# Performance work log

Measured on AMD Instinct MI355X. Metric: run time of the kernel, lower is better.

Reference implementation:

```python
import jax, jax.numpy as jnp
import numpy as np

DIM = 512
HEADS = 16
WS = 8          # window size
SHIFT = 4       # shift size
POSMLP = 32
MLP_HID = 4 * DIM
B = 32
HH = 56
WW = 56
EPS = 1e-5


def setup_inputs() -> dict:
    key = jax.random.key(0)
    ks = jax.random.split(key, 20)
    s = 0.02
    inp = {
        'x': jax.random.normal(ks[0], (B, HH * WW, DIM), jnp.float32),
        'g1': jnp.ones((DIM,), jnp.float32),
        'be1': jnp.zeros((DIM,), jnp.float32),
        'w_qkv': s * jax.random.normal(ks[1], (3 * DIM, DIM), jnp.float32),
        'b_qkv': jnp.zeros((3 * DIM,), jnp.float32),
        'pm_w1': s * jax.random.normal(ks[2], (POSMLP, 2), jnp.float32),
        'pm_b1': jnp.zeros((POSMLP,), jnp.float32),
        'pm_w2': s * jax.random.normal(ks[3], (HEADS, POSMLP), jnp.float32),
        'pm_b2': jnp.zeros((HEADS,), jnp.float32),
        'w_proj': s * jax.random.normal(ks[4], (DIM, DIM), jnp.float32),
        'b_proj': jnp.zeros((DIM,), jnp.float32),
        'g2': jnp.ones((DIM,), jnp.float32),
        'be2': jnp.zeros((DIM,), jnp.float32),
        'w_fc1': s * jax.random.normal(ks[5], (MLP_HID, DIM), jnp.float32),
        'b_fc1': jnp.zeros((MLP_HID,), jnp.float32),
        'w_fc2': s * jax.random.normal(ks[6], (DIM, MLP_HID), jnp.float32),
        'b_fc2': jnp.zeros((DIM,), jnp.float32),
        'H': HH,
        'W': WW,
    }
    return inp


def _layernorm(x, g, b):
    m = jnp.mean(x, -1, keepdims=True)
    v = jnp.mean(jnp.square(x - m), -1, keepdims=True)
    return (x - m) * jax.lax.rsqrt(v + EPS) * g + b


def _shift_mask(H, W, ws, sh):
    # static numpy construction of the (nW, N, N) 0/-100 shift mask
    img = np.zeros((H, W), np.float32)
    cnt = 0
    for hs in (slice(0, -ws), slice(-ws, -sh), slice(-sh, None)):
        for wsl in (slice(0, -ws), slice(-ws, -sh), slice(-sh, None)):
            img[hs, wsl] = cnt
            cnt += 1
    mw = img.reshape(H // ws, ws, W // ws, ws).transpose(0, 2, 1, 3).reshape(-1, ws * ws)
    diff = mw[:, None, :] - mw[:, :, None]
    return jnp.asarray(np.where(diff != 0, -100.0, 0.0).astype(np.float32))


def _pos_bias(ws, pm_w1, pm_b1, pm_w2, pm_b2):
    # log-CPB relative position bias computed by a tiny MLP -> (heads, N, N)
    g = jnp.stack(jnp.meshgrid(jnp.arange(ws), jnp.arange(ws), indexing='ij'))
    coords = g.reshape(2, -1).astype(jnp.float32)        # [2, N]
    d = coords[:, :, None] - coords[:, None, :]          # [2, N, N]
    d = jnp.sign(d) * jnp.log1p(jnp.abs(d))
    h = jax.nn.relu(jnp.einsum('cnm,oc->onm', d, pm_w1) + pm_b1[:, None, None])
    return jnp.einsum('onm,ho->hnm', h, pm_w2) + pm_b2[:, None, None]


def reference(x, g1, be1, w_qkv, b_qkv, pm_w1, pm_b1, pm_w2, pm_b2,
              w_proj, b_proj, g2, be2, w_fc1, b_fc1, w_fc2, b_fc2, H, W):
    ws, sh, nh = WS, SHIFT, HEADS
    Bb, L, C = x.shape
    hd = C // nh
    scale = hd ** -0.5
    N = ws * ws
    nWh, nWw = H // ws, W // ws
    nW = nWh * nWw

    shortcut = x
    xn = _layernorm(x, g1, be1).reshape(Bb, H, W, C)
    xn = jnp.roll(xn, (-sh, -sh), axis=(1, 2))
    # window partition -> (B*nW, N, C)
    xw = xn.reshape(Bb, nWh, ws, nWw, ws, C).transpose(0, 1, 3, 2, 4, 5).reshape(-1, N, C)

    qkv = (xw @ w_qkv.T + b_qkv).reshape(-1, N, 3, nh, hd).transpose(2, 0, 3, 1, 4)
    q, k, v = qkv[0], qkv[1], qkv[2]           # each (B*nW, nh, N, hd)

    attn = jnp.einsum('bhnd,bhmd->bhnm', q * scale, k)
    attn = attn + _pos_bias(ws, pm_w1, pm_b1, pm_w2, pm_b2)[None]

    mask = _shift_mask(H, W, ws, sh)           # (nW, N, N)
    attn = attn.reshape(Bb, nW, nh, N, N) + mask[None, :, None]
    attn = jax.nn.softmax(attn.reshape(-1, nh, N, N), axis=-1)

    out = jnp.einsum('bhnm,bhmd->bhnd', attn, v).transpose(0, 2, 1, 3).reshape(-1, N, C)
    out = out @ w_proj.T + b_proj

    # window reverse + roll back
    out = out.reshape(Bb, nWh, nWw, ws, ws, C).transpose(0, 1, 3, 2, 4, 5).reshape(Bb, H, W, C)
    out = jnp.roll(out, (sh, sh), axis=(1, 2)).reshape(Bb, L, C)

    x1 = shortcut + out
    h = jax.nn.gelu(_layernorm(x1, g2, be2) @ w_fc1.T + b_fc1, approximate=False)
    return x1 + (h @ w_fc2.T + b_fc2)
```

## Files before the change

### kernel.cpp

```cpp
#include <hip/hip_runtime.h>
#include <math.h>

typedef __bf16 bf16;
typedef bf16 bf16x8 __attribute__((ext_vector_type(8)));
typedef float f32x4 __attribute__((ext_vector_type(4)));

#define MFMA_BF16(a, b, c) __builtin_amdgcn_mfma_f32_16x16x32_bf16((a), (b), (c), 0, 0, 0)
#define GLDS16(gp, lp)                                                            \
  __builtin_amdgcn_global_load_lds((__attribute__((address_space(1))) void*)(gp), \
                                   (__attribute__((address_space(3))) void*)(lp), 16, 0, 0)
#define VMCNT4 asm volatile("s_waitcnt vmcnt(4)" ::: "memory")
#define LGKM0 asm volatile("s_waitcnt lgkmcnt(0)" ::: "memory")
#define SBAR __builtin_amdgcn_s_barrier()
#define SCHED0 __builtin_amdgcn_sched_barrier(0)

static constexpr int kDim   = 512;
static constexpr int kHeads = 16;
static constexpr int kHd    = 32;
static constexpr int kNt    = 64;
static constexpr int kNw    = 49;
static constexpr int kL     = 3136;
static constexpr int kToks  = 100352;
static constexpr int kWins  = 1568;
static constexpr int kHid   = 2048;
static constexpr size_t kQS = (size_t)kWins * kHeads * kNt * kHd;

__global__ __launch_bounds__(256) void wconv_kernel(const float* __restrict__ s,
                                                    bf16* __restrict__ d, int n8) {
  int i = blockIdx.x * 256 + threadIdx.x;
  if (i >= n8) return;
  const float4 a = *(const float4*)(s + i * 8);
  const float4 b = *(const float4*)(s + i * 8 + 4);
  bf16x8 o;
  o[0] = (bf16)a.x; o[1] = (bf16)a.y; o[2] = (bf16)a.z; o[3] = (bf16)a.w;
  o[4] = (bf16)b.x; o[5] = (bf16)b.y; o[6] = (bf16)b.z; o[7] = (bf16)b.w;
  *(bf16x8*)(d + i * 8) = o;
}

__global__ void posbias_kernel(const float* __restrict__ w1, const float* __restrict__ b1,
                               const float* __restrict__ w2, const float* __restrict__ b2,
                               float* __restrict__ tbl) {
  int idx = blockIdx.x * 256 + threadIdx.x;
  if (idx >= kHeads * kNt * kNt) return;
  int h = idx >> 12, n = (idx >> 6) & 63, m = idx & 63;
  float dr = (float)((n >> 3) - (m >> 3));
  float dc = (float)((n & 7) - (m & 7));
  dr = (dr > 0.f ? 1.f : (dr < 0.f ? -1.f : 0.f)) * log1pf(fabsf(dr));
  dc = (dc > 0.f ? 1.f : (dc < 0.f ? -1.f : 0.f)) * log1pf(fabsf(dc));
  float acc = b2[h];
  for (int o = 0; o < 32; ++o) {
    float hv = w1[o * 2] * dr + w1[o * 2 + 1] * dc + b1[o];
    acc += w2[h * 32 + o] * fmaxf(hv, 0.f);
  }
  tbl[idx] = acc;
}

template <int MODE>
__global__ __launch_bounds__(256) void ln_kernel(const float* __restrict__ x,
                                                 const float* __restrict__ g,
                                                 const float* __restrict__ be,
                                                 bf16* __restrict__ o) {
  const int t = blockIdx.x * 4 + (threadIdx.x >> 6);
  const int lane = threadIdx.x & 63;
  size_t src;
  if (MODE == 0) {
    const int win = t >> 6, n = t & 63;
    const int b = win / kNw, wi = win % kNw;
    const int h0 = ((wi / 7) * 8 + (n >> 3) + 4) % 56;
    const int w0 = ((wi % 7) * 8 + (n & 7) + 4) % 56;
    src = ((size_t)b * kL + h0 * 56 + w0) * kDim;
  } else {
    src = (size_t)t * kDim;
  }
  const float4 a = *(const float4*)(x + src + lane * 8);
  const float4 bq = *(const float4*)(x + src + lane * 8 + 4);
  float xf[8] = {a.x, a.y, a.z, a.w, bq.x, bq.y, bq.z, bq.w};
  float s = 0.f, s2 = 0.f;
#pragma unroll
  for (int j = 0; j < 8; ++j) { s += xf[j]; s2 += xf[j] * xf[j]; }
#pragma unroll
  for (int off = 32; off > 0; off >>= 1) { s += __shfl_xor(s, off); s2 += __shfl_xor(s2, off); }
  const float mean = s * (1.f / 512.f);
  const float rstd = rsqrtf(s2 * (1.f / 512.f) - mean * mean + 1e-5f);
  const float4 ga = *(const float4*)(g + lane * 8);
  const float4 gb = *(const float4*)(g + lane * 8 + 4);
  const float4 ba = *(const float4*)(be + lane * 8);
  const float4 bb = *(const float4*)(be + lane * 8 + 4);
  const float gv[8] = {ga.x, ga.y, ga.z, ga.w, gb.x, gb.y, gb.z, gb.w};
  const float bv[8] = {ba.x, ba.y, ba.z, ba.w, bb.x, bb.y, bb.z, bb.w};
  bf16x8 ov;
#pragma unroll
  for (int j = 0; j < 8; ++j) ov[j] = (bf16)((xf[j] - mean) * rstd * gv[j] + bv[j]);
  *(bf16x8*)(o + (size_t)t * kDim + lane * 8) = ov;
}

#define READ_A(KH, MB)                                             \
  _Pragma("unroll") for (int i = 0; i < 4; ++i)                    \
      af[i] = *(const bf16x8*)(&L[cb][0][KH][aoff + (MB + i) * 512]);
#define READ_B(KH)                                                 \
  _Pragma("unroll") for (int i = 0; i < 4; ++i)                    \
      bfr[i] = *(const bf16x8*)(&L[cb][1][KH][boff + i * 512]);
#define MFMAS(MB)                                                  \
  LGKM0;                                                           \
  SCHED0;                                                          \
  __builtin_amdgcn_s_setprio(1);                                   \
  _Pragma("unroll") for (int mi = 0; mi < 4; ++mi)                 \
  _Pragma("unroll") for (int ni = 0; ni < 4; ++ni)                 \
      acc[MB + mi][ni] = MFMA_BF16(af[mi], bfr[ni], acc[MB + mi][ni]); \
  __builtin_amdgcn_s_setprio(0)

template <int EPI>
__global__ __launch_bounds__(512, 1) void gemm256(const bf16* __restrict__ A, const bf16* __restrict__ B,
                                                  const float* __restrict__ bias, void* __restrict__ Cv,
                                                  const float* __restrict__ extra, int N, int K) {
  __shared__ __align__(16) bf16 L[2][2][2][8192];
  const int nbn = N >> 8;
  const int nwg = (int)gridDim.x;
  int wg = (int)blockIdx.x;
  {
    const int q = nwg >> 3, r = nwg & 7;
    const int xcd = wg & 7, loc = wg >> 3;
    wg = (xcd < r ? xcd * (q + 1) : r * (q + 1) + (xcd - r) * q) + loc;
  }
  const int bm = wg / nbn, bn = wg % nbn;
  const int tid = (int)threadIdx.x;
  const int wave = tid >> 6, lane = tid & 63;
  const int wm2 = wave >> 2, wn4 = wave & 3;
  const int quad = lane >> 4, l16 = lane & 15;

  const int sl0 = tid, sl1 = 512 + tid;
  const int rp0 = sl0 >> 3, ls0 = (sl0 & 7) ^ (rp0 & 7);
  const int rp1 = sl1 >> 3, ls1 = (sl1 & 7) ^ (rp1 & 7);
  const int row0 = rp0 * 2 + (ls0 >> 2), c0 = ls0 & 3;
  const int row1 = rp1 * 2 + (ls1 >> 2), c1 = ls1 & 3;
  const bf16* pa0 = A + (size_t)(bm * 256 + row0) * K + c0 * 8;
  const bf16* pa1 = A + (size_t)(bm * 256 + row1) * K + c1 * 8;
  const bf16* pb0 = B + (size_t)(bn * 256 + row0) * K + c0 * 8;
  const bf16* pb1 = B + (size_t)(bn * 256 + row1) * K + c1 * 8;

  const int ar = wm2 * 128 + l16, arp = ar >> 1;
  const int aoff = (arp * 8 + ((((ar & 1) << 2) | quad) ^ (arp & 7))) * 8;
  const int br = wn4 * 64 + l16, brp = br >> 1;
  const int boff = (brp * 8 + ((((br & 1) << 2) | quad) ^ (brp & 7))) * 8;

  f32x4 acc[8][4] = {};
  bf16x8 af[4], bfr[4];

  GLDS16(pa0, &L[0][0][0][sl0 * 8]);
  GLDS16(pa1, &L[0][0][0][sl1 * 8]);
  GLDS16(pb0, &L[0][1][0][sl0 * 8]);
  GLDS16(pb1, &L[0][1][0][sl1 * 8]);
  GLDS16(pa0 + 32, &L[0][0][1][sl0 * 8]);
  GLDS16(pa1 + 32, &L[0][0][1][sl1 * 8]);
  GLDS16(pb0 + 32, &L[0][1][1][sl0 * 8]);
  GLDS16(pb1 + 32, &L[0][1][1][sl1 * 8]);
  VMCNT4;
  SBAR;

#pragma unroll 2
  for (int kt = 0; kt < K; kt += 64) {
    const int cb = (kt >> 6) & 1, nb = cb ^ 1;
    const int kn = (kt + 64 < K) ? (kt + 64) : kt;
    READ_A(0, 0);
    READ_B(0);
    GLDS16(pa0 + kn, &L[nb][0][0][sl0 * 8]);
    GLDS16(pa1 + kn, &L[nb][0][0][sl1 * 8]);
    SBAR;
    MFMAS(0);
    SBAR;
    READ_A(0, 4);
    GLDS16(pb0 + kn, &L[nb][1][0][sl0 * 8]);
    GLDS16(pb1 + kn, &L[nb][1][0][sl1 * 8]);
    SBAR;
    MFMAS(4);
    VMCNT4;
    SBAR;
    READ_A(1, 0);
    READ_B(1);
    GLDS16(pa0 + kn + 32, &L[nb][0][1][sl0 * 8]);
    GLDS16(pa1 + kn + 32, &L[nb][0][1][sl1 * 8]);
    SBAR;
    MFMAS(0);
    SBAR;
    READ_A(1, 4);
    GLDS16(pb0 + kn + 32, &L[nb][1][1][sl0 * 8]);
    GLDS16(pb1 + kn + 32, &L[nb][1][1][sl1 * 8]);
    SBAR;
    MFMAS(4);
    VMCNT4;
    SBAR;
  }

  bf16* Cb = (bf16*)Cv;
  float* Cf = (float*)Cv;
#pragma unroll
  for (int mi = 0; mi < 8; ++mi) {
#pragma unroll
    for (int ni = 0; ni < 4; ++ni) {
      const int col = bn * 256 + wn4 * 64 + ni * 16 + l16;
      const float bb = bias[col];
#pragma unroll
      for (int r = 0; r < 4; ++r) {
        const int row = bm * 256 + wm2 * 128 + mi * 16 + quad * 4 + r;
        float val = acc[mi][ni][r] + bb;
        if constexpr (EPI == 1) {
          const int which = col >> 9, head = (col >> 5) & 15, d = col & 31;
          const int win = row >> 6, n = row & 63;
          Cb[(size_t)which * kQS + (((size_t)win * kHeads + head) * kNt + n) * kHd + d] = (bf16)val;
        } else if constexpr (EPI == 2) {
          val = 0.5f * val * (1.f + erff(val * 0.70710678118654752f));
          Cb[(size_t)row * N + col] = (bf16)val;
        } else if constexpr (EPI == 3) {
          Cf[(size_t)row * N + col] = val + extra[(size_t)row * N + col];
        } else {
          const int win = row >> 6, n = row & 63;
          const int b = win / kNw, wi = win % kNw;
          const int h0 = ((wi / 7) * 8 + (n >> 3) + 4) % 56;
          const int w0 = ((wi % 7) * 8 + (n & 7) + 4) % 56;
          const size_t dst = ((size_t)b * kL + h0 * 56 + w0) * kDim + col;
          Cf[dst] = val + extra[dst];
        }
      }
    }
  }
}

__device__ __forceinline__ int reg3(int x) { return x < 48 ? 0 : (x < 52 ? 1 : 2); }

__global__ __launch_bounds__(128) void attn_kernel(const bf16* __restrict__ qkv,
                                                   const float* __restrict__ ptbl,
                                                   bf16* __restrict__ out) {
  __shared__ float Sb[2][64 * 65];
  __shared__ float Rs[2][64];
  __shared__ bf16  Pb[2][64 * 72];
  __shared__ bf16  Vt[2][32 * 72];
  const int w = threadIdx.x >> 6, lane = threadIdx.x & 63;
  const int gwh = blockIdx.x * 2 + w;
  const int win = gwh >> 4, h = gwh & 15;
  const int quad = lane >> 4, l16 = lane & 15;
  const bf16* q = qkv + ((size_t)win * kHeads + h) * (kNt * kHd);
  const bf16* k = q + kQS;
  const bf16* v = q + 2 * kQS;

#pragma unroll
  for (int i = 0; i < 4; ++i) {
    const int row = i * 16 + (lane >> 2);
    const int d0 = (lane & 3) * 8;
    bf16x8 vv = *(const bf16x8*)(v + row * kHd + d0);
#pragma unroll
    for (int j = 0; j < 8; ++j) Vt[w][(d0 + j) * 72 + row] = vv[j];
  }

  bf16x8 qf[4], kf[4];
#pragma unroll
  for (int i = 0; i < 4; ++i) qf[i] = *(const bf16x8*)(q + (i * 16 + l16) * kHd + quad * 8);
#pragma unroll
  for (int j = 0; j < 4; ++j) kf[j] = *(const bf16x8*)(k + (j * 16 + l16) * kHd + quad * 8);
  f32x4 sa[4][4] = {};
#pragma unroll
  for (int i = 0; i < 4; ++i)
#pragma unroll
    for (int j = 0; j < 4; ++j) sa[i][j] = MFMA_BF16(qf[i], kf[j], sa[i][j]);

  const int wi = win % kNw;
  const int hb = (wi / 7) * 8, wb = (wi % 7) * 8;
  const float* bh = ptbl + h * 4096;
#pragma unroll
  for (int i = 0; i < 4; ++i) {
#pragma unroll
    for (int j = 0; j < 4; ++j) {
      const int ct = j * 16 + l16;
      const int crg = reg3(hb + (ct >> 3)) * 3 + reg3(wb + (ct & 7));
#pragma unroll
      for (int r = 0; r < 4; ++r) {
        const int rt = i * 16 + quad * 4 + r;
        const int rrg = reg3(hb + (rt >> 3)) * 3 + reg3(wb + (rt & 7));
        float sv = sa[i][j][r] * 0.17677669529663687f + bh[rt * 64 + ct];
        if (rrg != crg) sv -= 100.f;
        Sb[w][rt * 65 + ct] = sv;
      }
    }
  }
  __syncthreads();

  float mx = -1e30f;
  for (int i = 0; i < 64; ++i) mx = fmaxf(mx, Sb[w][lane * 65 + i]);
  float sum = 0.f;
  for (int i = 0; i < 64; ++i) {
    const float p = __expf(Sb[w][lane * 65 + i] - mx);
    sum += p;
    Pb[w][lane * 72 + i] = (bf16)p;
  }
  Rs[w][lane] = 1.f / sum;
  __syncthreads();

  f32x4 oa[4][2] = {};
#pragma unroll
  for (int kk = 0; kk < 2; ++kk) {
    bf16x8 pf[4], vf[2];
#pragma unroll
    for (int mi = 0; mi < 4; ++mi)
      pf[mi] = *(const bf16x8*)(&Pb[w][(mi * 16 + l16) * 72 + kk * 32 + quad * 8]);
#pragma unroll
    for (int nj = 0; nj < 2; ++nj)
      vf[nj] = *(const bf16x8*)(&Vt[w][(nj * 16 + l16) * 72 + kk * 32 + quad * 8]);
#pragma unroll
    for (int mi = 0; mi < 4; ++mi)
#pragma unroll
      for (int nj = 0; nj < 2; ++nj) oa[mi][nj] = MFMA_BF16(pf[mi], vf[nj], oa[mi][nj]);
  }
#pragma unroll
  for (int mi = 0; mi < 4; ++mi)
#pragma unroll
    for (int nj = 0; nj < 2; ++nj)
#pragma unroll
      for (int r = 0; r < 4; ++r) {
        const int row = mi * 16 + quad * 4 + r;
        const int col = nj * 16 + l16;
        out[((size_t)win * kNt + row) * kDim + h * kHd + col] = (bf16)(oa[mi][nj][r] * Rs[w][row]);
      }
}

extern "C" void kernel_launch(void* const* d_in, const int* in_sizes, int n_in,
                              void* d_out, int out_size, void* d_ws, size_t ws_size,
                              hipStream_t stream) {
  (void)in_sizes; (void)n_in; (void)out_size; (void)ws_size;
  const float* x      = (const float*)d_in[0];
  const float* g1     = (const float*)d_in[1];
  const float* be1    = (const float*)d_in[2];
  const float* w_qkv  = (const float*)d_in[3];
  const float* b_qkv  = (const float*)d_in[4];
  const float* pm_w1  = (const float*)d_in[5];
  const float* pm_b1  = (const float*)d_in[6];
  const float* pm_w2  = (const float*)d_in[7];
  const float* pm_b2  = (const float*)d_in[8];
  const float* w_proj = (const float*)d_in[9];
  const float* b_proj = (const float*)d_in[10];
  const float* g2     = (const float*)d_in[11];
  const float* be2    = (const float*)d_in[12];
  const float* w_fc1  = (const float*)d_in[13];
  const float* b_fc1  = (const float*)d_in[14];
  const float* w_fc2  = (const float*)d_in[15];
  const float* b_fc2  = (const float*)d_in[16];
  float* out = (float*)d_out;
  char* ws = (char*)d_ws;

  constexpr size_t OFF_WB   = 1u << 20;
  constexpr size_t OFF_XW   = OFF_WB + (8u << 20);
  constexpr size_t SZ_ACT   = (size_t)kToks * kDim * 2;
  constexpr size_t OFF_QKV  = OFF_XW + SZ_ACT;
  float* biastbl = (float*)ws;
  bf16* wqb = (bf16*)(ws + OFF_WB);
  bf16* wpb = wqb + 786432;
  bf16* w1b = wpb + 262144;
  bf16* w2b = w1b + 1048576;
  bf16* xw    = (bf16*)(ws + OFF_XW);
  bf16* attnb = xw;
  bf16* xn2   = xw;
  bf16* qkvb = (bf16*)(ws + OFF_QKV);
  float* x1  = (float*)(ws + OFF_QKV);
  bf16* hbuf = (bf16*)(ws + OFF_QKV + (size_t)kToks * kDim * 4);

  wconv_kernel<<<dim3(786432 / 2048), dim3(256), 0, stream>>>(w_qkv, wqb, 786432 / 8);
  wconv_kernel<<<dim3(262144 / 2048), dim3(256), 0, stream>>>(w_proj, wpb, 262144 / 8);
  wconv_kernel<<<dim3(1048576 / 2048), dim3(256), 0, stream>>>(w_fc1, w1b, 1048576 / 8);
  wconv_kernel<<<dim3(1048576 / 2048), dim3(256), 0, stream>>>(w_fc2, w2b, 1048576 / 8);
  posbias_kernel<<<dim3(256), dim3(256), 0, stream>>>(pm_w1, pm_b1, pm_w2, pm_b2, biastbl);
  ln_kernel<0><<<dim3(kToks / 4), dim3(256), 0, stream>>>(x, g1, be1, xw);
  gemm256<1><<<dim3((kToks / 256) * (1536 / 256)), dim3(512), 0, stream>>>(
      xw, wqb, b_qkv, qkvb, nullptr, 1536, 512);
  attn_kernel<<<dim3(kWins * kHeads / 2), dim3(128), 0, stream>>>(qkvb, biastbl, attnb);
  gemm256<4><<<dim3((kToks / 256) * (512 / 256)), dim3(512), 0, stream>>>(
      attnb, wpb, b_proj, x1, x, 512, 512);
  ln_kernel<1><<<dim3(kToks / 4), dim3(256), 0, stream>>>(x1, g2, be2, xn2);
  constexpr int kChunk = kToks / 4;
  for (int c = 0; c < 4; ++c) {
    const size_t ro = (size_t)c * kChunk * kDim;
    gemm256<2><<<dim3((kChunk / 256) * (kHid / 256)), dim3(512), 0, stream>>>(
        xn2 + ro, w1b, b_fc1, hbuf, nullptr, kHid, 512);
    gemm256<3><<<dim3((kChunk / 256) * (512 / 256)), dim3(512), 0, stream>>>(
        hbuf, w2b, b_fc2, out + ro, x1 + ro, 512, kHid);
  }
}
```

Baseline: 1.660 ms.

## Double-buffer GEMM register fragments and relax waits to overlap LDS reads with MFMA

Restructures the 256x256 GEMM main loop so LDS fragment reads for the next MFMA group are issued before the current group runs, using two register sets and partial lgkmcnt/vmcnt waits instead of full drains. Several barriers are removed to cut stalls between the LDS reads and the MFMA work. It also changes launch bounds to request two workgroups per CU, which limits registers per thread and risks spills. The finer-grained waits also add risk that some data hazard has been overlooked.

```diff
diff --git a/kernel.cpp b/kernel.cpp
--- a/kernel.cpp
+++ b/kernel.cpp
@@ -9,8 +9,8 @@
 #define GLDS16(gp, lp)                                                            \
   __builtin_amdgcn_global_load_lds((__attribute__((address_space(1))) void*)(gp), \
                                    (__attribute__((address_space(3))) void*)(lp), 16, 0, 0)
-#define VMCNT4 asm volatile("s_waitcnt vmcnt(4)" ::: "memory")
-#define LGKM0 asm volatile("s_waitcnt lgkmcnt(0)" ::: "memory")
+#define VMCNT(N) asm volatile("s_waitcnt vmcnt(" #N ")" ::: "memory")
+#define LGKM(N) asm volatile("s_waitcnt lgkmcnt(" #N ")" ::: "memory")
 #define SBAR __builtin_amdgcn_s_barrier()
 #define SCHED0 __builtin_amdgcn_sched_barrier(0)
 
@@ -94,23 +94,22 @@
   *(bf16x8*)(o + (size_t)t * kDim + lane * 8) = ov;
 }
 
-#define READ_A(KH, MB)                                             \
-  _Pragma("unroll") for (int i = 0; i < 4; ++i)                    \
-      af[i] = *(const bf16x8*)(&L[cb][0][KH][aoff + (MB + i) * 512]);
-#define READ_B(KH)                                                 \
-  _Pragma("unroll") for (int i = 0; i < 4; ++i)                    \
-      bfr[i] = *(const bf16x8*)(&L[cb][1][KH][boff + i * 512]);
-#define MFMAS(MB)                                                  \
-  LGKM0;                                                           \
-  SCHED0;                                                          \
-  __builtin_amdgcn_s_setprio(1);                                   \
-  _Pragma("unroll") for (int mi = 0; mi < 4; ++mi)                 \
-  _Pragma("unroll") for (int ni = 0; ni < 4; ++ni)                 \
-      acc[MB + mi][ni] = MFMA_BF16(af[mi], bfr[ni], acc[MB + mi][ni]); \
+#define LOAD_A(dst, CB, KH, MB)                                        \
+  _Pragma("unroll") for (int i = 0; i < 4; ++i)                        \
+      dst[i] = *(const bf16x8*)(&L[CB][0][KH][aoff + (MB + i) * 512]);
+#define LOAD_B(dst, CB, KH)                                            \
+  _Pragma("unroll") for (int i = 0; i < 4; ++i)                        \
+      dst[i] = *(const bf16x8*)(&L[CB][1][KH][boff + i * 512]);
+#define MFMAS(MB, AF, BF)                                              \
+  SCHED0;                                                              \
+  __builtin_amdgcn_s_setprio(1);                                       \
+  _Pragma("unroll") for (int mi = 0; mi < 4; ++mi)                     \
+  _Pragma("unroll") for (int ni = 0; ni < 4; ++ni)                     \
+      acc[MB + mi][ni] = MFMA_BF16(AF[mi], BF[ni], acc[MB + mi][ni]);  \
   __builtin_amdgcn_s_setprio(0)
 
 template <int EPI>
-__global__ __launch_bounds__(512, 1) void gemm256(const bf16* __restrict__ A, const bf16* __restrict__ B,
+__global__ __launch_bounds__(512, 2) void gemm256(const bf16* __restrict__ A, const bf16* __restrict__ B,
                                                   const float* __restrict__ bias, void* __restrict__ Cv,
                                                   const float* __restrict__ extra, int N, int K) {
   __shared__ __align__(16) bf16 L[2][2][2][8192];
@@ -144,7 +143,7 @@
   const int boff = (brp * 8 + ((((br & 1) << 2) | quad) ^ (brp & 7))) * 8;
 
   f32x4 acc[8][4] = {};
-  bf16x8 af[4], bfr[4];
+  bf16x8 af0[4], af1[4], bfr0[4], bfr1[4];
 
   GLDS16(pa0, &L[0][0][0][sl0 * 8]);
   GLDS16(pa1, &L[0][0][0][sl1 * 8]);
@@ -154,40 +153,42 @@
   GLDS16(pa1 + 32, &L[0][0][1][sl1 * 8]);
   GLDS16(pb0 + 32, &L[0][1][1][sl0 * 8]);
   GLDS16(pb1 + 32, &L[0][1][1][sl1 * 8]);
-  VMCNT4;
+  VMCNT(4);
   SBAR;
+  LOAD_A(af0, 0, 0, 0);
+  LOAD_B(bfr0, 0, 0);
 
 #pragma unroll 2
   for (int kt = 0; kt < K; kt += 64) {
     const int cb = (kt >> 6) & 1, nb = cb ^ 1;
     const int kn = (kt + 64 < K) ? (kt + 64) : kt;
-    READ_A(0, 0);
-    READ_B(0);
+    LOAD_A(af1, cb, 0, 4);
     GLDS16(pa0 + kn, &L[nb][0][0][sl0 * 8]);
     GLDS16(pa1 + kn, &L[nb][0][0][sl1 * 8]);
+    LGKM(4);
+    MFMAS(0, af0, bfr0);
+    VMCNT(2);
     SBAR;
-    MFMAS(0);
-    SBAR;
-    READ_A(0, 4);
+    LOAD_A(af0, cb, 1, 0);
+    LOAD_B(bfr1, cb, 1);
     GLDS16(pb0 + kn, &L[nb][1][0][sl0 * 8]);
     GLDS16(pb1 + kn, &L[nb][1][0][sl1 * 8]);
+    LGKM(8);
+    MFMAS(4, af1, bfr0);
     SBAR;
-    MFMAS(4);
-    VMCNT4;
-    SBAR;
-    READ_A(1, 0);
-    READ_B(1);
+    LOAD_A(af1, cb, 1, 4);
     GLDS16(pa0 + kn + 32, &L[nb][0][1][sl0 * 8]);
     GLDS16(pa1 + kn + 32, &L[nb][0][1][sl1 * 8]);
+    LGKM(4);
+    MFMAS(0, af0, bfr1);
+    VMCNT(2);
     SBAR;
-    MFMAS(0);
-    SBAR;
-    READ_A(1, 4);
+    LOAD_A(af0, nb, 0, 0);
+    LOAD_B(bfr0, nb, 0);
     GLDS16(pb0 + kn + 32, &L[nb][1][1][sl0 * 8]);
     GLDS16(pb1 + kn + 32, &L[nb][1][1][sl1 * 8]);
-    SBAR;
-    MFMAS(4);
-    VMCNT4;
+    LGKM(8);
+    MFMAS(4, af1, bfr1);
     SBAR;
   }
 
```

After: 1.683 ms. About the same (+1.4%).
